# Performance work log

Measured on AMD Instinct MI355X. Metric: run time of the kernel, lower is better.

The kernel has to match this reference:

```python
import jax, jax.numpy as jnp
import numpy as np
import math

HIDDEN = 768
LABEL_NUM = 16
N_HEADS = 12
HEAD_DIM = HIDDEN // N_HEADS


def setup_inputs() -> dict:
    key = jax.random.key(0)
    ks = jax.random.split(key, 8)
    B, S, L, Ls, H = 8, 128, LABEL_NUM, 8, HIDDEN
    std = 1.0 / math.sqrt(H)
    return {
        "token_embs": jax.random.normal(ks[0], (B, S, H), jnp.float32),
        "label_embs": jax.random.normal(ks[1], (L, Ls, H), jnp.float32),
        "token_mask": jnp.ones((B, S), jnp.float32),
        "label_mask": jnp.ones((L, Ls), jnp.float32),
        "Wq": jax.random.normal(ks[2], (H, H), jnp.float32) * std,
        "bq": jnp.zeros((H,), jnp.float32),
        "Wk": jax.random.normal(ks[3], (H, H), jnp.float32) * std,
        "bk": jnp.zeros((H,), jnp.float32),
        "Wv": jax.random.normal(ks[4], (H, H), jnp.float32) * std,
        "bv": jnp.zeros((H,), jnp.float32),
    }


def reference(token_embs, label_embs, token_mask, label_mask, Wq, bq, Wk, bk, Wv, bv):
    B, S, H = token_embs.shape
    L, Ls, _ = label_embs.shape
    T = S + Ls
    # broadcast (instead of repeat) then concat: [B, L, T, H] -> [B*L, T, H]
    tok = jnp.broadcast_to(token_embs[:, None, :, :], (B, L, S, H))
    lab = jnp.broadcast_to(label_embs[None, :, :, :], (B, L, Ls, H))
    x = jnp.concatenate([tok, lab], axis=2).reshape(B * L, T, H)
    # mask: [B*L, T]; extended additive mask (1-m)*-10000
    tm = jnp.broadcast_to(token_mask[:, None, :], (B, L, S))
    lm = jnp.broadcast_to(label_mask[None, :, :], (B, L, Ls))
    mask = jnp.concatenate([tm, lm], axis=2).reshape(B * L, T)
    bias = (1.0 - mask) * -10000.0  # [BL, T]
    # QKV (torch Linear: y = x W^T + b)
    q = (x @ Wq.T + bq).reshape(B * L, T, N_HEADS, HEAD_DIM)
    k = (x @ Wk.T + bk).reshape(B * L, T, N_HEADS, HEAD_DIM)
    v = (x @ Wv.T + bv).reshape(B * L, T, N_HEADS, HEAD_DIM)
    scores = jnp.einsum("bthd,bshd->bhts", q, k) / math.sqrt(HEAD_DIM)
    scores = scores + bias[:, None, None, :]
    probs = jax.nn.softmax(scores, axis=-1)
    ctx = jnp.einsum("bhts,bshd->bthd", probs, v).reshape(B * L, T, H)
    # [B, L, T, H] -> [B, T, L, H]
    fused = ctx.reshape(B, L, T, H).transpose(0, 2, 1, 3)
    return (fused,)
```

## Files before the change

kernel.cpp:

```cpp
#include <hip/hip_runtime.h>
#include <hip/hip_bf16.h>
#include <stdint.h>

#define HIDDEN 768
#define NH 12
#define HD 64
#define BB 8
#define SS 128
#define LL 16
#define LS 8
#define TT 136
#define NROWS 1152
#define BH (BB * NH)

typedef __attribute__((ext_vector_type(8))) short bf16x8;
typedef __attribute__((ext_vector_type(4))) float f32x4;
typedef __attribute__((ext_vector_type(16))) float f32x16;
typedef __hip_bfloat16 bf16;

__device__ inline float tof(bf16 x) { return __bfloat162float(x); }
__device__ inline uint16_t b16bits(float f) {
    bf16 h = __float2bfloat16(f);
    union { bf16 h; uint16_t u; } u; u.h = h; return u.u;
}

__global__ __launch_bounds__(256) void qkv_kernel(
    const float* __restrict__ tok, const float* __restrict__ lab,
    const float* __restrict__ Wq, const float* __restrict__ bq,
    const float* __restrict__ Wk, const float* __restrict__ bk,
    const float* __restrict__ Wv, const float* __restrict__ bv,
    bf16* __restrict__ Qw, bf16* __restrict__ Kw, bf16* __restrict__ Vw)
{
    __shared__ __align__(16) uint16_t As[2][64 * 40];
    __shared__ __align__(16) uint16_t Bs[2][128 * 40];

    int tid = threadIdx.x;
    int lane = tid & 63, wv = tid >> 6;
    int ml = lane & 15, quad = lane >> 4;
    int mt = blockIdx.x / 18, nt = blockIdx.x % 18;
    int wr = wv >> 1, wc = wv & 1;

    int mat = nt / 6;
    int col0 = (nt % 6) * 128;
    const float* wbase = (mat == 0) ? Wq : ((mat == 1) ? Wk : Wv);
    const float* bptr  = (mat == 0) ? bq : ((mat == 1) ? bk : bv);
    bf16* obase        = (mat == 0) ? Qw : ((mat == 1) ? Kw : Vw);

    int ar0 = mt * 64;
    const float* asrc = (ar0 < 1024) ? (tok + (size_t)ar0 * HIDDEN)
                                     : (lab + (size_t)(ar0 - 1024) * HIDDEN);
    const float* bsrc = wbase + (size_t)col0 * HIDDEN;

    int ra_r[2], ra_c[2], rb_r[4], rb_c[4];
    #pragma unroll
    for (int i = 0; i < 2; ++i) { int gi = i * 256 + tid; ra_r[i] = gi >> 3; ra_c[i] = (gi & 7) * 4; }
    #pragma unroll
    for (int i = 0; i < 4; ++i) { int gi = i * 256 + tid; rb_r[i] = gi >> 3; rb_c[i] = (gi & 7) * 4; }

    float4 ra[2], rb[4];
    #pragma unroll
    for (int i = 0; i < 2; ++i)
        ra[i] = *reinterpret_cast<const float4*>(asrc + (size_t)ra_r[i] * HIDDEN + ra_c[i]);
    #pragma unroll
    for (int i = 0; i < 4; ++i)
        rb[i] = *reinterpret_cast<const float4*>(bsrc + (size_t)rb_r[i] * HIDDEN + rb_c[i]);

    f32x4 acc[2][4] = {};
    int p = 0;

    for (int k0 = 0; k0 < HIDDEN; k0 += 32) {
        #pragma unroll
        for (int i = 0; i < 2; ++i) {
            ushort4 hh;
            hh.x = b16bits(ra[i].x); hh.y = b16bits(ra[i].y);
            hh.z = b16bits(ra[i].z); hh.w = b16bits(ra[i].w);
            *reinterpret_cast<ushort4*>(&As[p][ra_r[i] * 40 + ra_c[i]]) = hh;
        }
        #pragma unroll
        for (int i = 0; i < 4; ++i) {
            ushort4 hh;
            hh.x = b16bits(rb[i].x); hh.y = b16bits(rb[i].y);
            hh.z = b16bits(rb[i].z); hh.w = b16bits(rb[i].w);
            *reinterpret_cast<ushort4*>(&Bs[p][rb_r[i] * 40 + rb_c[i]]) = hh;
        }
        __syncthreads();

        if (k0 + 32 < HIDDEN) {
            #pragma unroll
            for (int i = 0; i < 2; ++i)
                ra[i] = *reinterpret_cast<const float4*>(asrc + (size_t)ra_r[i] * HIDDEN + k0 + 32 + ra_c[i]);
            #pragma unroll
            for (int i = 0; i < 4; ++i)
                rb[i] = *reinterpret_cast<const float4*>(bsrc + (size_t)rb_r[i] * HIDDEN + k0 + 32 + rb_c[i]);
        }

        bf16x8 af[2], bfr[4];
        #pragma unroll
        for (int rt = 0; rt < 2; ++rt)
            af[rt] = *reinterpret_cast<const bf16x8*>(&As[p][(wr * 32 + rt * 16 + ml) * 40 + quad * 8]);
        #pragma unroll
        for (int ct = 0; ct < 4; ++ct)
            bfr[ct] = *reinterpret_cast<const bf16x8*>(&Bs[p][(wc * 64 + ct * 16 + ml) * 40 + quad * 8]);
        #pragma unroll
        for (int rt = 0; rt < 2; ++rt)
            #pragma unroll
            for (int ct = 0; ct < 4; ++ct)
                acc[rt][ct] = __builtin_amdgcn_mfma_f32_16x16x32_bf16(af[rt], bfr[ct], acc[rt][ct], 0, 0, 0);
        p ^= 1;
    }

    #pragma unroll
    for (int ct = 0; ct < 4; ++ct) {
        int c = col0 + wc * 64 + ct * 16 + ml;
        float bvv = bptr[c];
        #pragma unroll
        for (int rt = 0; rt < 2; ++rt) {
            #pragma unroll
            for (int reg = 0; reg < 4; ++reg) {
                int R = mt * 64 + wr * 32 + rt * 16 + quad * 4 + reg;
                obase[(size_t)R * HIDDEN + c] = __float2bfloat16(acc[rt][ct][reg] + bvv);
            }
        }
    }
}

__global__ __launch_bounds__(256) void attn_tt_kernel(
    const bf16* __restrict__ Qw, const bf16* __restrict__ Kw,
    const bf16* __restrict__ Vw, const float* __restrict__ tmask,
    bf16* __restrict__ ctx_tt, float* __restrict__ m_tt, float* __restrict__ d_tt)
{
    __shared__ __align__(16) uint32_t KldsW[128 * 36];
    __shared__ __align__(16) uint32_t VtW[64 * 68];
    __shared__ __align__(16) uint32_t PW[4][16 * 68];
    __shared__ float bias_s[128];

    int bh = blockIdx.x >> 1;
    int hf = blockIdx.x & 1;
    int b = bh / NH, h = bh % NH;
    int tid = threadIdx.x;
    int lane = tid & 63, wv = tid >> 6;
    int ml = lane & 15, quad = lane >> 4;

    for (int i = tid; i < 128 * 32; i += 256) {
        int s = i >> 5, w = i & 31;
        KldsW[s * 36 + w] =
            reinterpret_cast<const uint32_t*>(Kw + (size_t)(b * SS + s) * HIDDEN + h * HD)[w];
    }
    for (int i = tid; i < 64 * 64; i += 256) {
        int d = i & 63, s2 = i >> 6;
        const uint16_t* v0 = reinterpret_cast<const uint16_t*>(Vw + (size_t)(b * SS + 2 * s2) * HIDDEN + h * HD);
        const uint16_t* v1 = reinterpret_cast<const uint16_t*>(Vw + (size_t)(b * SS + 2 * s2 + 1) * HIDDEN + h * HD);
        VtW[d * 68 + s2] = (uint32_t)v0[d] | ((uint32_t)v1[d] << 16);
    }
    for (int i = tid; i < 128; i += 256)
        bias_s[i] = (1.0f - tmask[b * SS + i]) * -10000.0f;
    __syncthreads();

    const bf16* Klb = reinterpret_cast<const bf16*>(KldsW);
    const bf16* Vtb = reinterpret_cast<const bf16*>(VtW);
    const bf16* Pb  = reinterpret_cast<const bf16*>(PW[wv]);

    int qr = hf * 64 + wv * 16 + ml;
    const bf16* qp = Qw + (size_t)(b * SS + qr) * HIDDEN + h * HD + quad * 8;
    bf16x8 a0 = *reinterpret_cast<const bf16x8*>(qp);
    bf16x8 a1 = *reinterpret_cast<const bf16x8*>(qp + 32);

    f32x4 sc[8];
    #pragma unroll
    for (int ct = 0; ct < 8; ++ct) {
        const bf16* kp = Klb + (ct * 16 + ml) * 72 + quad * 8;
        bf16x8 b0 = *reinterpret_cast<const bf16x8*>(kp);
        bf16x8 b1 = *reinterpret_cast<const bf16x8*>(kp + 32);
        f32x4 z = {0.f, 0.f, 0.f, 0.f};
        z = __builtin_amdgcn_mfma_f32_16x16x32_bf16(a0, b0, z, 0, 0, 0);
        z = __builtin_amdgcn_mfma_f32_16x16x32_bf16(a1, b1, z, 0, 0, 0);
        sc[ct] = z;
    }

    float mx[4] = {-1e30f, -1e30f, -1e30f, -1e30f};
    #pragma unroll
    for (int ct = 0; ct < 8; ++ct) {
        float bc = bias_s[ct * 16 + ml];
        #pragma unroll
        for (int reg = 0; reg < 4; ++reg) {
            float v = sc[ct][reg] * 0.125f + bc;
            sc[ct][reg] = v;
            mx[reg] = fmaxf(mx[reg], v);
        }
    }
    #pragma unroll
    for (int reg = 0; reg < 4; ++reg)
        #pragma unroll
        for (int off = 1; off < 16; off <<= 1)
            mx[reg] = fmaxf(mx[reg], __shfl_xor(mx[reg], off));

    float Zs[4] = {0.f, 0.f, 0.f, 0.f};
    #pragma unroll
    for (int ct = 0; ct < 8; ++ct) {
        #pragma unroll
        for (int reg = 0; reg < 4; ++reg) {
            float e = __expf(sc[ct][reg] - mx[reg]);
            sc[ct][reg] = e;
            Zs[reg] += e;
        }
    }
    #pragma unroll
    for (int reg = 0; reg < 4; ++reg)
        #pragma unroll
        for (int off = 1; off < 16; off <<= 1)
            Zs[reg] += __shfl_xor(Zs[reg], off);

    #pragma unroll
    for (int reg = 0; reg < 4; ++reg) {
        int gr = bh * 128 + hf * 64 + wv * 16 + quad * 4 + reg;
        if (ml == 0) { m_tt[gr] = mx[reg]; d_tt[gr] = Zs[reg]; }
    }

    #pragma unroll
    for (int ct = 0; ct < 8; ++ct) {
        #pragma unroll
        for (int reg = 0; reg < 4; ++reg) {
            float e = sc[ct][reg];
            float ep = __shfl_xor(e, 1);
            if ((ml & 1) == 0)
                PW[wv][(quad * 4 + reg) * 68 + ct * 8 + (ml >> 1)] =
                    (uint32_t)b16bits(e) | ((uint32_t)b16bits(ep) << 16);
        }
    }

    float rZ[4];
    #pragma unroll
    for (int reg = 0; reg < 4; ++reg) rZ[reg] = 1.0f / Zs[reg];

    #pragma unroll
    for (int ct4 = 0; ct4 < 4; ++ct4) {
        f32x4 acc = {0.f, 0.f, 0.f, 0.f};
        #pragma unroll
        for (int ks = 0; ks < 4; ++ks) {
            bf16x8 ap = *reinterpret_cast<const bf16x8*>(Pb + ml * 136 + ks * 32 + quad * 8);
            bf16x8 bp = *reinterpret_cast<const bf16x8*>(Vtb + (ct4 * 16 + ml) * 136 + ks * 32 + quad * 8);
            acc = __builtin_amdgcn_mfma_f32_16x16x32_bf16(ap, bp, acc, 0, 0, 0);
        }
        #pragma unroll
        for (int reg = 0; reg < 4; ++reg) {
            int gr = bh * 128 + hf * 64 + wv * 16 + quad * 4 + reg;
            ctx_tt[(size_t)gr * 64 + ct4 * 16 + ml] = __float2bfloat16(acc[reg] * rZ[reg]);
        }
    }
}

__global__ __launch_bounds__(256) void attn_merge_kernel(
    const bf16* __restrict__ Qw, const bf16* __restrict__ Kw,
    const bf16* __restrict__ Vw,
    const bf16* __restrict__ ctx_tt, const float* __restrict__ m_tt,
    const float* __restrict__ d_tt,
    const float* __restrict__ tmask, const float* __restrict__ lmask,
    float* __restrict__ out)
{
    __shared__ __align__(16) uint32_t VtW[64 * 84];
    __shared__ __align__(16) uint32_t PWL[16 * 84];
    __shared__ __align__(16) uint32_t P2W[4][32 * 8];
    __shared__ float wtab[4][32], itab[4][32];
    __shared__ float mtt_s[128], dtt_s[128], bias_t[128];
    __shared__ float bias_l[16];

    int p = blockIdx.x & 7;
    int h = (blockIdx.x >> 3) % NH;
    int b = blockIdx.x / (8 * NH);
    int l0 = 2 * p, l1 = l0 + 1;
    int bh = b * NH + h;
    int tid = threadIdx.x;
    int lane = tid & 63, wv = tid >> 6;
    int ml = lane & 15, quad = lane >> 4;
    int hl = lane & 31, hi = lane >> 5;

    for (int i = tid; i < 64 * 80; i += 256) {
        int d = i & 63, s2 = i >> 6;
        uint32_t w = 0;
        #pragma unroll
        for (int half = 0; half < 2; ++half) {
            int s = 2 * s2 + half;
            int row = -1;
            if (s < 128)      row = b * SS + s;
            else if (s < 136) row = 1024 + l0 * LS + (s - 128);
            else if (s < 144) row = 1024 + l1 * LS + (s - 136);
            uint16_t v = 0;
            if (row >= 0)
                v = reinterpret_cast<const uint16_t*>(Vw + (size_t)row * HIDDEN + h * HD)[d];
            w |= (uint32_t)v << (16 * half);
        }
        VtW[d * 84 + s2] = w;
    }
    if (tid < 128) {
        mtt_s[tid] = m_tt[bh * 128 + tid];
        dtt_s[tid] = d_tt[bh * 128 + tid];
        bias_t[tid] = (1.0f - tmask[b * SS + tid]) * -10000.0f;
    }
    if (tid < 16) {
        int labk = (tid < 8) ? (l0 * LS + tid) : (l1 * LS + tid - 8);
        bias_l[tid] = (1.0f - lmask[labk]) * -10000.0f;
    }
    if (tid < 128)
        PWL[(tid >> 3) * 84 + 72 + (tid & 7)] = 0;
    __syncthreads();

    const bf16* Vtb = reinterpret_cast<const bf16*>(VtW);

    int kprow = 1024 + ((ml < 8) ? (l0 * LS + ml) : (l1 * LS + ml - 8));
    const bf16* kpp = Kw + (size_t)kprow * HIDDEN + h * HD + quad * 8;
    bf16x8 kb0 = *reinterpret_cast<const bf16x8*>(kpp);
    bf16x8 kb1 = *reinterpret_cast<const bf16x8*>(kpp + 32);

    if (wv < 3) {
        const bf16* P2b = reinterpret_cast<const bf16*>(P2W[wv]);
        for (int rt = wv; rt < 8; rt += 3) {
            int tq = rt * 16 + ml;
            const bf16* qp = Qw + (size_t)(b * SS + tq) * HIDDEN + h * HD + quad * 8;
            bf16x8 a0 = *reinterpret_cast<const bf16x8*>(qp);
            bf16x8 a1 = *reinterpret_cast<const bf16x8*>(qp + 32);

            f32x4 z = {0.f, 0.f, 0.f, 0.f};
            z = __builtin_amdgcn_mfma_f32_16x16x32_bf16(a0, kb0, z, 0, 0, 0);
            z = __builtin_amdgcn_mfma_f32_16x16x32_bf16(a1, kb1, z, 0, 0, 0);

            #pragma unroll
            for (int reg = 0; reg < 4; ++reg) {
                int trow = quad * 4 + reg;
                float s = z[reg] * 0.125f + bias_l[ml];
                float m = s;
                m = fmaxf(m, __shfl_xor(m, 1));
                m = fmaxf(m, __shfl_xor(m, 2));
                m = fmaxf(m, __shfl_xor(m, 4));
                float mtt = mtt_s[rt * 16 + trow], dtt = dtt_s[rt * 16 + trow];
                float m_new = fmaxf(mtt, m);
                float e = __expf(s - m_new);
                float dh = e;
                dh += __shfl_xor(dh, 1);
                dh += __shfl_xor(dh, 2);
                dh += __shfl_xor(dh, 4);
                float alpha = __expf(mtt - m_new);
                float w = alpha * dtt;
                float inv = 1.0f / (w + dh);
                if (ml == 0) { wtab[wv][trow] = w;      itab[wv][trow] = inv; }
                if (ml == 8) { wtab[wv][16 + trow] = w; itab[wv][16 + trow] = inv; }
                float ep = __shfl_xor(e, 1);
                if ((ml & 1) == 0) {
                    uint32_t pk = (uint32_t)b16bits(e) | ((uint32_t)b16bits(ep) << 16);
                    P2W[wv][trow * 8 + (ml >> 1)]        = (ml < 8) ? pk : 0u;
                    P2W[wv][(16 + trow) * 8 + (ml >> 1)] = (ml < 8) ? 0u : pk;
                }
            }

            bf16x8 ap  = *reinterpret_cast<const bf16x8*>(P2b + hl * 16 + hi * 8);
            bf16x8 bv0 = *reinterpret_cast<const bf16x8*>(Vtb + hl * 168 + 128 + hi * 8);
            bf16x8 bv1 = *reinterpret_cast<const bf16x8*>(Vtb + (32 + hl) * 168 + 128 + hi * 8);
            f32x16 c0 = {}, c1 = {};
            c0 = __builtin_amdgcn_mfma_f32_32x32x16_bf16(ap, bv0, c0, 0, 0, 0);
            c1 = __builtin_amdgcn_mfma_f32_32x32x16_bf16(ap, bv1, c1, 0, 0, 0);

            float cv0[8], cv1[8];
            #pragma unroll
            for (int reg = 0; reg < 8; ++reg) {
                int row = (reg & 3) + 8 * (reg >> 2) + 4 * hi;
                const bf16* cp = ctx_tt + (size_t)(bh * 128 + rt * 16 + row) * 64;
                cv0[reg] = tof(cp[hl]);
                cv1[reg] = tof(cp[32 + hl]);
            }
            #pragma unroll
            for (int reg = 0; reg < 16; ++reg) {
                int row = (reg & 3) + 8 * (reg >> 2) + 4 * hi;
                int trow = row & 15;
                int lsel = (row < 16) ? l0 : l1;
                float w = wtab[wv][row], inv = itab[wv][row];
                float c0v = (reg < 8) ? cv0[reg] : cv0[reg - 8];
                float c1v = (reg < 8) ? cv1[reg] : cv1[reg - 8];
                size_t ob = (((size_t)b * TT + rt * 16 + trow) * LL + lsel) * HIDDEN + h * HD;
                out[ob + hl]      = (w * c0v + c0[reg]) * inv;
                out[ob + 32 + hl] = (w * c1v + c1[reg]) * inv;
            }
        }
    } else {
        const bf16* Pb = reinterpret_cast<const bf16*>(PWL);
        int qrow = 1024 + ((ml < 8) ? (l0 * LS + ml) : (l1 * LS + ml - 8));
        const bf16* qp = Qw + (size_t)qrow * HIDDEN + h * HD + quad * 8;
        bf16x8 a0 = *reinterpret_cast<const bf16x8*>(qp);
        bf16x8 a1 = *reinterpret_cast<const bf16x8*>(qp + 32);

        f32x4 sc[9];
        #pragma unroll
        for (int ct = 0; ct < 9; ++ct) {
            bf16x8 b0, b1;
            if (ct < 8) {
                const bf16* kp = Kw + (size_t)(b * SS + ct * 16 + ml) * HIDDEN + h * HD + quad * 8;
                b0 = *reinterpret_cast<const bf16x8*>(kp);
                b1 = *reinterpret_cast<const bf16x8*>(kp + 32);
            } else { b0 = kb0; b1 = kb1; }
            f32x4 zz = {0.f, 0.f, 0.f, 0.f};
            zz = __builtin_amdgcn_mfma_f32_16x16x32_bf16(a0, b0, zz, 0, 0, 0);
            zz = __builtin_amdgcn_mfma_f32_16x16x32_bf16(a1, b1, zz, 0, 0, 0);
            sc[ct] = zz;
        }

        float mx[4] = {-1e30f, -1e30f, -1e30f, -1e30f};
        #pragma unroll
        for (int ct = 0; ct < 9; ++ct) {
            #pragma unroll
            for (int reg = 0; reg < 4; ++reg) {
                int rq = quad * 4 + reg;
                float bc = (ct < 8) ? bias_t[ct * 16 + ml]
                                    : (((rq < 8) != (ml < 8)) ? -1e30f : bias_l[ml]);
                float v = sc[ct][reg] * 0.125f + bc;
                sc[ct][reg] = v;
                mx[reg] = fmaxf(mx[reg], v);
            }
        }
        #pragma unroll
        for (int reg = 0; reg < 4; ++reg)
            #pragma unroll
            for (int off = 1; off < 16; off <<= 1)
                mx[reg] = fmaxf(mx[reg], __shfl_xor(mx[reg], off));

        float Zs[4] = {0.f, 0.f, 0.f, 0.f};
        #pragma unroll
        for (int ct = 0; ct < 9; ++ct) {
            #pragma unroll
            for (int reg = 0; reg < 4; ++reg) {
                float e = __expf(sc[ct][reg] - mx[reg]);
                sc[ct][reg] = e;
                Zs[reg] += e;
            }
        }
        #pragma unroll
        for (int reg = 0; reg < 4; ++reg)
            #pragma unroll
            for (int off = 1; off < 16; off <<= 1)
                Zs[reg] += __shfl_xor(Zs[reg], off);
        float zi[4];
        #pragma unroll
        for (int reg = 0; reg < 4; ++reg) zi[reg] = 1.0f / Zs[reg];

        #pragma unroll
        for (int ct = 0; ct < 9; ++ct) {
            #pragma unroll
            for (int reg = 0; reg < 4; ++reg) {
                float e = sc[ct][reg];
                float ep = __shfl_xor(e, 1);
                if ((ml & 1) == 0)
                    PWL[(quad * 4 + reg) * 84 + ct * 8 + (ml >> 1)] =
                        (uint32_t)b16bits(e) | ((uint32_t)b16bits(ep) << 16);
            }
        }

        #pragma unroll
        for (int ct4 = 0; ct4 < 4; ++ct4) {
            f32x4 acc = {0.f, 0.f, 0.f, 0.f};
            #pragma unroll
            for (int ks = 0; ks < 5; ++ks) {
                bf16x8 ap = *reinterpret_cast<const bf16x8*>(Pb + ml * 168 + ks * 32 + quad * 8);
                bf16x8 bp = *reinterpret_cast<const bf16x8*>(Vtb + (ct4 * 16 + ml) * 168 + ks * 32 + quad * 8);
                acc = __builtin_amdgcn_mfma_f32_16x16x32_bf16(ap, bp, acc, 0, 0, 0);
            }
            #pragma unroll
            for (int reg = 0; reg < 4; ++reg) {
                int rq = quad * 4 + reg;
                int l = (rq < 8) ? l0 : l1;
                int t = SS + (rq & 7);
                out[(((size_t)b * TT + t) * LL + l) * HIDDEN + h * HD + ct4 * 16 + ml] =
                    acc[reg] * zi[reg];
            }
        }
    }
}

extern "C" void kernel_launch(void* const* d_in, const int* in_sizes, int n_in,
                              void* d_out, int out_size, void* d_ws, size_t ws_size,
                              hipStream_t stream)
{
    const float* tok   = (const float*)d_in[0];
    const float* lab   = (const float*)d_in[1];
    const float* tmask = (const float*)d_in[2];
    const float* lmask = (const float*)d_in[3];
    const float* Wq    = (const float*)d_in[4];
    const float* bq    = (const float*)d_in[5];
    const float* Wk    = (const float*)d_in[6];
    const float* bk    = (const float*)d_in[7];
    const float* Wv    = (const float*)d_in[8];
    const float* bv    = (const float*)d_in[9];

    bf16* Qw = (bf16*)d_ws;
    bf16* Kw = Qw + (size_t)NROWS * HIDDEN;
    bf16* Vw = Kw + (size_t)NROWS * HIDDEN;
    bf16* ctx = Vw + (size_t)NROWS * HIDDEN;
    float* m_tt = (float*)(ctx + (size_t)BH * 128 * 64);
    float* d_tt = m_tt + BH * 128;

    qkv_kernel<<<dim3(18 * 18), 256, 0, stream>>>(
        tok, lab, Wq, bq, Wk, bk, Wv, bv, Qw, Kw, Vw);
    attn_tt_kernel<<<dim3(BH * 2), 256, 0, stream>>>(
        Qw, Kw, Vw, tmask, ctx, m_tt, d_tt);
    attn_merge_kernel<<<dim3(BB * NH * 8), 256, 0, stream>>>(
        Qw, Kw, Vw, ctx, m_tt, d_tt, tmask, lmask, (float*)d_out);
}
```

Before: 138.2 us.

## Widen QKV K-tile to 64, vectorize V transpose, share transposed V via global

The QKV GEMM now stages 64-wide K slices per iteration instead of 32, halving the barrier count at the cost of more LDS and registers. The attention token-token kernel loads V with 32-bit words when transposing into LDS, and the first half-block writes the transposed V tile to a new global buffer. The merge kernel then copies that pre-transposed tile instead of doing its own scattered 16-bit transposing gathers, and builds only the label columns itself. This adds a global write/read round trip and more workspace, and relies on kernel ordering on the stream for correctness.

```diff
diff --git a/kernel.cpp b/kernel.cpp
--- a/kernel.cpp
+++ b/kernel.cpp
@@ -31,8 +31,8 @@
     const float* __restrict__ Wv, const float* __restrict__ bv,
     bf16* __restrict__ Qw, bf16* __restrict__ Kw, bf16* __restrict__ Vw)
 {
-    __shared__ __align__(16) uint16_t As[2][64 * 40];
-    __shared__ __align__(16) uint16_t Bs[2][128 * 40];
+    __shared__ __align__(16) uint16_t As[2][64 * 72];
+    __shared__ __align__(16) uint16_t Bs[2][128 * 72];
 
     int tid = threadIdx.x;
     int lane = tid & 63, wv = tid >> 6;
@@ -51,61 +51,64 @@
                                      : (lab + (size_t)(ar0 - 1024) * HIDDEN);
     const float* bsrc = wbase + (size_t)col0 * HIDDEN;
 
-    int ra_r[2], ra_c[2], rb_r[4], rb_c[4];
-    #pragma unroll
-    for (int i = 0; i < 2; ++i) { int gi = i * 256 + tid; ra_r[i] = gi >> 3; ra_c[i] = (gi & 7) * 4; }
-    #pragma unroll
-    for (int i = 0; i < 4; ++i) { int gi = i * 256 + tid; rb_r[i] = gi >> 3; rb_c[i] = (gi & 7) * 4; }
-
-    float4 ra[2], rb[4];
-    #pragma unroll
-    for (int i = 0; i < 2; ++i)
+    int ra_r[4], ra_c[4], rb_r[8], rb_c[8];
+    #pragma unroll
+    for (int i = 0; i < 4; ++i) { int gi = i * 256 + tid; ra_r[i] = gi >> 4; ra_c[i] = (gi & 15) * 4; }
+    #pragma unroll
+    for (int i = 0; i < 8; ++i) { int gi = i * 256 + tid; rb_r[i] = gi >> 4; rb_c[i] = (gi & 15) * 4; }
+
+    float4 ra[4], rb[8];
+    #pragma unroll
+    for (int i = 0; i < 4; ++i)
         ra[i] = *reinterpret_cast<const float4*>(asrc + (size_t)ra_r[i] * HIDDEN + ra_c[i]);
     #pragma unroll
-    for (int i = 0; i < 4; ++i)
+    for (int i = 0; i < 8; ++i)
         rb[i] = *reinterpret_cast<const float4*>(bsrc + (size_t)rb_r[i] * HIDDEN + rb_c[i]);
 
     f32x4 acc[2][4] = {};
     int p = 0;
 
-    for (int k0 = 0; k0 < HIDDEN; k0 += 32) {
-        #pragma unroll
-        for (int i = 0; i < 2; ++i) {
+    for (int k0 = 0; k0 < HIDDEN; k0 += 64) {
+        #pragma unroll
+        for (int i = 0; i < 4; ++i) {
             ushort4 hh;
             hh.x = b16bits(ra[i].x); hh.y = b16bits(ra[i].y);
             hh.z = b16bits(ra[i].z); hh.w = b16bits(ra[i].w);
-            *reinterpret_cast<ushort4*>(&As[p][ra_r[i] * 40 + ra_c[i]]) = hh;
-        }
-        #pragma unroll
-        for (int i = 0; i < 4; ++i) {
+            *reinterpret_cast<ushort4*>(&As[p][ra_r[i] * 72 + ra_c[i]]) = hh;
+        }
+        #pragma unroll
+        for (int i = 0; i < 8; ++i) {
             ushort4 hh;
             hh.x = b16bits(rb[i].x); hh.y = b16bits(rb[i].y);
             hh.z = b16bits(rb[i].z); hh.w = b16bits(rb[i].w);
-            *reinterpret_cast<ushort4*>(&Bs[p][rb_r[i] * 40 + rb_c[i]]) = hh;
+            *reinterpret_cast<ushort4*>(&Bs[p][rb_r[i] * 72 + rb_c[i]]) = hh;
         }
         __syncthreads();
 
-        if (k0 + 32 < HIDDEN) {
-            #pragma unroll
-            for (int i = 0; i < 2; ++i)
-                ra[i] = *reinterpret_cast<const float4*>(asrc + (size_t)ra_r[i] * HIDDEN + k0 + 32 + ra_c[i]);
+        if (k0 + 64 < HIDDEN) {
             #pragma unroll
             for (int i = 0; i < 4; ++i)
-                rb[i] = *reinterpret_cast<const float4*>(bsrc + (size_t)rb_r[i] * HIDDEN + k0 + 32 + rb_c[i]);
-        }
-
-        bf16x8 af[2], bfr[4];
-        #pragma unroll
-        for (int rt = 0; rt < 2; ++rt)
-            af[rt] = *reinterpret_cast<const bf16x8*>(&As[p][(wr * 32 + rt * 16 + ml) * 40 + quad * 8]);
-        #pragma unroll
-        for (int ct = 0; ct < 4; ++ct)
-            bfr[ct] = *reinterpret_cast<const bf16x8*>(&Bs[p][(wc * 64 + ct * 16 + ml) * 40 + quad * 8]);
-        #pragma unroll
-        for (int rt = 0; rt < 2; ++rt)
+                ra[i] = *reinterpret_cast<const float4*>(asrc + (size_t)ra_r[i] * HIDDEN + k0 + 64 + ra_c[i]);
+            #pragma unroll
+            for (int i = 0; i < 8; ++i)
+                rb[i] = *reinterpret_cast<const float4*>(bsrc + (size_t)rb_r[i] * HIDDEN + k0 + 64 + rb_c[i]);
+        }
+
+        #pragma unroll
+        for (int kh = 0; kh < 2; ++kh) {
+            bf16x8 af[2], bfr[4];
+            #pragma unroll
+            for (int rt = 0; rt < 2; ++rt)
+                af[rt] = *reinterpret_cast<const bf16x8*>(&As[p][(wr * 32 + rt * 16 + ml) * 72 + kh * 32 + quad * 8]);
             #pragma unroll
             for (int ct = 0; ct < 4; ++ct)
-                acc[rt][ct] = __builtin_amdgcn_mfma_f32_16x16x32_bf16(af[rt], bfr[ct], acc[rt][ct], 0, 0, 0);
+                bfr[ct] = *reinterpret_cast<const bf16x8*>(&Bs[p][(wc * 64 + ct * 16 + ml) * 72 + kh * 32 + quad * 8]);
+            #pragma unroll
+            for (int rt = 0; rt < 2; ++rt)
+                #pragma unroll
+                for (int ct = 0; ct < 4; ++ct)
+                    acc[rt][ct] = __builtin_amdgcn_mfma_f32_16x16x32_bf16(af[rt], bfr[ct], acc[rt][ct], 0, 0, 0);
+        }
         p ^= 1;
     }
 
@@ -127,7 +130,8 @@
 __global__ __launch_bounds__(256) void attn_tt_kernel(
     const bf16* __restrict__ Qw, const bf16* __restrict__ Kw,
     const bf16* __restrict__ Vw, const float* __restrict__ tmask,
-    bf16* __restrict__ ctx_tt, float* __restrict__ m_tt, float* __restrict__ d_tt)
+    bf16* __restrict__ ctx_tt, float* __restrict__ m_tt, float* __restrict__ d_tt,
+    uint32_t* __restrict__ Vt_g)
 {
     __shared__ __align__(16) uint32_t KldsW[128 * 36];
     __shared__ __align__(16) uint32_t VtW[64 * 68];
@@ -146,15 +150,28 @@
         KldsW[s * 36 + w] =
             reinterpret_cast<const uint32_t*>(Kw + (size_t)(b * SS + s) * HIDDEN + h * HD)[w];
     }
-    for (int i = tid; i < 64 * 64; i += 256) {
-        int d = i & 63, s2 = i >> 6;
-        const uint16_t* v0 = reinterpret_cast<const uint16_t*>(Vw + (size_t)(b * SS + 2 * s2) * HIDDEN + h * HD);
-        const uint16_t* v1 = reinterpret_cast<const uint16_t*>(Vw + (size_t)(b * SS + 2 * s2 + 1) * HIDDEN + h * HD);
-        VtW[d * 68 + s2] = (uint32_t)v0[d] | ((uint32_t)v1[d] << 16);
+    #pragma unroll
+    for (int c = 0; c < 8; ++c) {
+        int g = c * 256 + tid;
+        int s2 = g >> 5, dw = g & 31;
+        const uint32_t* v0 = reinterpret_cast<const uint32_t*>(Vw + (size_t)(b * SS + 2 * s2) * HIDDEN + h * HD);
+        const uint32_t* v1 = reinterpret_cast<const uint32_t*>(Vw + (size_t)(b * SS + 2 * s2 + 1) * HIDDEN + h * HD);
+        uint32_t a = v0[dw], bb = v1[dw];
+        VtW[(2 * dw) * 68 + s2]     = (a & 0xffffu) | ((bb & 0xffffu) << 16);
+        VtW[(2 * dw + 1) * 68 + s2] = (a >> 16) | (bb & 0xffff0000u);
     }
     for (int i = tid; i < 128; i += 256)
         bias_s[i] = (1.0f - tmask[b * SS + i]) * -10000.0f;
     __syncthreads();
+
+    if (hf == 0) {
+        uint32_t* vg = Vt_g + (size_t)bh * 4096;
+        #pragma unroll
+        for (int c = 0; c < 16; ++c) {
+            int g = c * 256 + tid;
+            vg[g] = VtW[(g >> 6) * 68 + (g & 63)];
+        }
+    }
 
     const bf16* Klb = reinterpret_cast<const bf16*>(KldsW);
     const bf16* Vtb = reinterpret_cast<const bf16*>(VtW);
@@ -251,7 +268,7 @@
 
 __global__ __launch_bounds__(256) void attn_merge_kernel(
     const bf16* __restrict__ Qw, const bf16* __restrict__ Kw,
-    const bf16* __restrict__ Vw,
+    const bf16* __restrict__ Vw, const uint32_t* __restrict__ Vt_g,
     const bf16* __restrict__ ctx_tt, const float* __restrict__ m_tt,
     const float* __restrict__ d_tt,
     const float* __restrict__ tmask, const float* __restrict__ lmask,
@@ -274,23 +291,26 @@
     int ml = lane & 15, quad = lane >> 4;
     int hl = lane & 31, hi = lane >> 5;
 
-    for (int i = tid; i < 64 * 80; i += 256) {
-        int d = i & 63, s2 = i >> 6;
-        uint32_t w = 0;
-        #pragma unroll
-        for (int half = 0; half < 2; ++half) {
-            int s = 2 * s2 + half;
-            int row = -1;
-            if (s < 128)      row = b * SS + s;
-            else if (s < 136) row = 1024 + l0 * LS + (s - 128);
-            else if (s < 144) row = 1024 + l1 * LS + (s - 136);
-            uint16_t v = 0;
-            if (row >= 0)
-                v = reinterpret_cast<const uint16_t*>(Vw + (size_t)row * HIDDEN + h * HD)[d];
-            w |= (uint32_t)v << (16 * half);
-        }
-        VtW[d * 84 + s2] = w;
-    }
+    {
+        const uint32_t* vg = Vt_g + (size_t)bh * 4096;
+        #pragma unroll
+        for (int c = 0; c < 16; ++c) {
+            int g = c * 256 + tid;
+            VtW[(g >> 6) * 84 + (g & 63)] = vg[g];
+        }
+    }
+    for (int g = tid; g < 512; g += 256) {
+        int d = g >> 3, jj = g & 7;
+        int s0 = 128 + 2 * jj, s1 = s0 + 1;
+        int r0 = (s0 < 136) ? (1024 + l0 * LS + (s0 - 128)) : (1024 + l1 * LS + (s0 - 136));
+        int r1 = (s1 < 136) ? (1024 + l0 * LS + (s1 - 128)) : (1024 + l1 * LS + (s1 - 136));
+        uint16_t lo = reinterpret_cast<const uint16_t*>(Vw + (size_t)r0 * HIDDEN + h * HD)[d];
+        uint16_t hi2 = reinterpret_cast<const uint16_t*>(Vw + (size_t)r1 * HIDDEN + h * HD)[d];
+        VtW[d * 84 + 64 + jj] = (uint32_t)lo | ((uint32_t)hi2 << 16);
+    }
+    for (int g = tid; g < 512; g += 256)
+        VtW[(g >> 3) * 84 + 72 + (g & 7)] = 0;
+
     if (tid < 128) {
         mtt_s[tid] = m_tt[bh * 128 + tid];
         dtt_s[tid] = d_tt[bh * 128 + tid];
@@ -493,11 +513,12 @@
     bf16* ctx = Vw + (size_t)NROWS * HIDDEN;
     float* m_tt = (float*)(ctx + (size_t)BH * 128 * 64);
     float* d_tt = m_tt + BH * 128;
+    uint32_t* Vt_g = (uint32_t*)(d_tt + BH * 128);
 
     qkv_kernel<<<dim3(18 * 18), 256, 0, stream>>>(
         tok, lab, Wq, bq, Wk, bk, Wv, bv, Qw, Kw, Vw);
     attn_tt_kernel<<<dim3(BH * 2), 256, 0, stream>>>(
-        Qw, Kw, Vw, tmask, ctx, m_tt, d_tt);
+        Qw, Kw, Vw, tmask, ctx, m_tt, d_tt, Vt_g);
     attn_merge_kernel<<<dim3(BB * NH * 8), 256, 0, stream>>>(
-        Qw, Kw, Vw, ctx, m_tt, d_tt, tmask, lmask, (float*)d_out);
+        Qw, Kw, Vw, Vt_g, ctx, m_tt, d_tt, tmask, lmask, (float*)d_out);
 }
```

Result: faster. 131.4 us (-4.9%).
